# Optimization experiments

Measured on AMD Instinct MI355X. Metric: run time of the kernel, lower is better.

## Reference

```python
import jax, jax.numpy as jnp
import numpy as np

N = 100000        # n_nodes
E = 1600000       # n_edges (avg degree 16)
D = 64            # latent_dim_S
H = 64            # gcn_hidden_dim
EPS = 1e-5        # BatchNorm1d eps


def setup_inputs() -> dict:
    key = jax.random.key(0)
    ks = jax.random.split(key, 6)
    return {
        "edge_index": jax.random.randint(ks[0], (2, E), 0, N, dtype=jnp.int64),
        "u_S": jax.random.normal(ks[1], (N, D), dtype=jnp.float32),
        # GCNConv 1: latent_dim_S -> gcn_hidden_dim
        "w1": jax.random.normal(ks[2], (D, H), dtype=jnp.float32) / np.sqrt(D).astype(np.float32),
        "b1": jnp.zeros((H,), jnp.float32),
        # BatchNorm1d(H)
        "g1": jnp.ones((H,), jnp.float32),
        "beta1": jnp.zeros((H,), jnp.float32),
        # GCNConv 2: gcn_hidden_dim -> 2
        "w2": jax.random.normal(ks[3], (H, 2), dtype=jnp.float32) / np.sqrt(H).astype(np.float32),
        "b2": jnp.zeros((2,), jnp.float32),
        # BatchNorm1d(2)
        "g2": jnp.ones((2,), jnp.float32),
        "beta2": jnp.zeros((2,), jnp.float32),
    }


def reference(edge_index, u_S, w1, b1, g1, beta1, w2, b2, g2, beta2):
    n = u_S.shape[0]
    # PyG GCNConv: add self-loops, symmetric normalization D^-1/2 A D^-1/2
    loop = jnp.arange(n, dtype=edge_index.dtype)
    src = jnp.concatenate([edge_index[0], loop])  # [E+N]
    dst = jnp.concatenate([edge_index[1], loop])
    deg = jnp.zeros((n,), u_S.dtype).at[dst].add(1.0)   # in-degree incl. self-loop (>=1)
    dinv = jax.lax.rsqrt(deg)
    norm = dinv[src] * dinv[dst]                         # [E+N]

    def gcn_conv(x, w, b):
        h = x @ w                                        # transform first (PyG order)
        msg = h[src] * norm[:, None]                     # gather + scale
        out = jnp.zeros((n, h.shape[1]), h.dtype).at[dst].add(msg)  # scatter-add
        return out + b                                   # bias after aggregation

    def batchnorm(x, g, bt):
        m = x.mean(axis=0)
        v = x.var(axis=0)                                # biased variance (train mode)
        return g * (x - m) * jax.lax.rsqrt(v + EPS) + bt

    s = jax.nn.relu(batchnorm(gcn_conv(u_S, w1, b1), g1, beta1))
    s = batchnorm(gcn_conv(s, w2, b2), g2, beta2)
    # nn.Softmax() on 2D input defaults to dim=1
    return jax.nn.sigmoid(s), jax.nn.softmax(s, axis=1)
```

## Files before the change

### kernel.cpp

```cpp
#include <hip/hip_runtime.h>
#include <hip/hip_fp16.h>

#define N_NODES 100000
#define N_EDGES 1600000
#define BN_EPS 1e-5f

#define NBUCK 256
#define NPB   391
#define BCAP  8192
#define EPB_BIN 4096
#define NBLK_BIN ((N_EDGES + EPB_BIN - 1) / EPB_BIN)

#define OFF_GCUR   0
#define OFF_CNT    256
#define OFF_DINV   100352
#define OFF_OFFS   200448
#define OFF_EBUF   300544
#define OFF_STATS1 2397696
#define OFF_STATS2 2397824
#define OFF_HS1    2398016
#define OFF_BINNED OFF_HS1
#define OFF_OUT1   5598016
#define OFF_HS2    8798016
#define OFF_OUT2   8998016

typedef _Float16 f16x8 __attribute__((ext_vector_type(8)));
typedef float    f32x4 __attribute__((ext_vector_type(4)));

__device__ inline float4 cvt4(uint2 v) {
    __half2 a = *(__half2*)&v.x, b = *(__half2*)&v.y;
    float2 fa = __half22float2(a), fb = __half22float2(b);
    return make_float4(fa.x, fa.y, fb.x, fb.y);
}

__global__ __launch_bounds__(256) void k0_init(int* __restrict__ gcur,
                                               float* __restrict__ stats) {
    int t = threadIdx.x;
    gcur[t] = t * BCAP;
    if (t < 132) stats[t] = 0.f;
}

__global__ __launch_bounds__(256) void k_bin(
        const int* __restrict__ src, const int* __restrict__ dst,
        int* __restrict__ gcur, int* __restrict__ binned) {
    __shared__ int hist[NBUCK];
    __shared__ int lcur[NBUCK];
    int t = threadIdx.x, b = blockIdx.x;
    hist[t] = 0;
    __syncthreads();
    int e0 = b * EPB_BIN;
    int pkreg[16], bkreg[16];
#pragma unroll
    for (int i = 0; i < 16; ++i) {
        int e = e0 + t + i * 256;
        if (e < N_EDGES) {
            int s = src[e], d = dst[e];
            int bk = d / NPB;
            bkreg[i] = bk;
            pkreg[i] = s | ((d - bk * NPB) << 17);
            atomicAdd(&hist[bk], 1);
        } else bkreg[i] = -1;
    }
    __syncthreads();
    int h = hist[t];
    lcur[t] = (h > 0) ? atomicAdd(&gcur[t], h) : 0;
    __syncthreads();
#pragma unroll
    for (int i = 0; i < 16; ++i) {
        if (bkreg[i] >= 0) {
            int bk = bkreg[i];
            int pos = atomicAdd(&lcur[bk], 1);
            if (pos < (bk + 1) * BCAP)
                binned[pos] = pkreg[i];
        }
    }
}

__global__ __launch_bounds__(256) void k_csr(
        const int* __restrict__ gcur, const int* __restrict__ binned,
        int* __restrict__ cnt, float* __restrict__ dinv,
        int* __restrict__ offs, int* __restrict__ ebuf) {
    int b = blockIdx.x, t = threadIdx.x;
    int nb0 = b * NPB;
    int nn = min(NPB, N_NODES - nb0);
    __shared__ int lcnt[NPB];
    __shared__ int lcur[NPB];
    __shared__ int sc[512];
    for (int i = t; i < NPB; i += 256) lcnt[i] = 0;
    __syncthreads();
    int base = b * BCAP;
    int m = min(gcur[b] - base, BCAP);
    for (int j = t; j < m; j += 256)
        atomicAdd(&lcnt[((unsigned)binned[base + j]) >> 17], 1);
    __syncthreads();
    sc[t] = (t < NPB) ? lcnt[t] : 0;
    sc[256 + t] = (256 + t < NPB) ? lcnt[256 + t] : 0;
    __syncthreads();
    for (int off = 1; off < 512; off <<= 1) {
        int v0 = (t >= off) ? sc[t - off] : 0;
        int i1 = t + 256;
        int v1 = (i1 >= off) ? sc[i1 - off] : 0;
        __syncthreads();
        sc[t] += v0; sc[i1] += v1;
        __syncthreads();
    }
    for (int i = t; i < nn; i += 256) {
        int c = lcnt[i];
        int excl = sc[i] - c;
        lcur[i] = excl;
        offs[nb0 + i] = base + excl;
        cnt[nb0 + i] = c;
        dinv[nb0 + i] = rsqrtf((float)(1 + c));
    }
    __syncthreads();
    for (int j = t; j < m; j += 256) {
        unsigned v = (unsigned)binned[base + j];
        int pos = atomicAdd(&lcur[v >> 17], 1);
        ebuf[base + pos] = (int)(v & 0x1FFFFu);
    }
}

__global__ __launch_bounds__(256) void k3_xw1(
        const float* __restrict__ u, const float* __restrict__ w1g,
        const float* __restrict__ dinv, __half* __restrict__ hs1) {
    int t = threadIdx.x;
    int lane = t & 63, wid = t >> 6;
    int g = blockIdx.x * 4 + wid;
    if (g >= N_NODES / 16) return;
    int r = lane & 15, kb = lane >> 4;

    f16x8 bf[4][2];
#pragma unroll
    for (int ct = 0; ct < 4; ++ct) {
#pragma unroll
        for (int kh = 0; kh < 2; ++kh) {
            int c = ct * 16 + r;
            int k0 = kh * 32 + kb * 8;
            f16x8 b;
#pragma unroll
            for (int i = 0; i < 8; ++i) b[i] = (_Float16)w1g[(k0 + i) * 64 + c];
            bf[ct][kh] = b;
        }
    }

    const float* up = u + (size_t)g * 16 * 64;
    f16x8 af[2];
#pragma unroll
    for (int kh = 0; kh < 2; ++kh) {
        const float* p = up + r * 64 + kh * 32 + kb * 8;
        float4 v0 = *(const float4*)p;
        float4 v1 = *(const float4*)(p + 4);
        f16x8 a;
        a[0] = (_Float16)v0.x; a[1] = (_Float16)v0.y;
        a[2] = (_Float16)v0.z; a[3] = (_Float16)v0.w;
        a[4] = (_Float16)v1.x; a[5] = (_Float16)v1.y;
        a[6] = (_Float16)v1.z; a[7] = (_Float16)v1.w;
        af[kh] = a;
    }

    f32x4 acc[4];
#pragma unroll
    for (int ct = 0; ct < 4; ++ct) { acc[ct][0]=0.f; acc[ct][1]=0.f; acc[ct][2]=0.f; acc[ct][3]=0.f; }
#pragma unroll
    for (int ct = 0; ct < 4; ++ct) {
        acc[ct] = __builtin_amdgcn_mfma_f32_16x16x32_f16(af[0], bf[ct][0], acc[ct], 0, 0, 0);
        acc[ct] = __builtin_amdgcn_mfma_f32_16x16x32_f16(af[1], bf[ct][1], acc[ct], 0, 0, 0);
    }

    int r0 = g * 16;
    float4 dv = *(const float4*)&dinv[r0 + kb * 4];
    float dvv[4] = {dv.x, dv.y, dv.z, dv.w};
#pragma unroll
    for (int ct = 0; ct < 4; ++ct) {
#pragma unroll
        for (int reg = 0; reg < 4; ++reg) {
            int row = r0 + kb * 4 + reg;
            int col = ct * 16 + r;
            hs1[(size_t)row * 64 + col] = __float2half(acc[ct][reg] * dvv[reg]);
        }
    }
}

__global__ __launch_bounds__(256) void k_pull1(
        const int* __restrict__ offs, const int* __restrict__ cnt,
        const int* __restrict__ ebuf, const float* __restrict__ dinv,
        const __half* __restrict__ hs1, __half* __restrict__ out1) {
    int idx = blockIdx.x * blockDim.x + threadIdx.x;
    int d = idx >> 4, sub = idx & 15;
    if (d >= N_NODES) return;
    const uint2* h4 = (const uint2*)hs1;
    float4 acc = cvt4(h4[d * 16 + sub]);
    int base = offs[d], c = cnt[d];
    if (c > 0) {
        int s = ebuf[base];
        int j = 0;
        for (; j + 1 < c; ++j) {
            int s2 = ebuf[base + j + 1];
            float4 v = cvt4(h4[s * 16 + sub]);
            acc.x += v.x; acc.y += v.y; acc.z += v.z; acc.w += v.w;
            s = s2;
        }
        float4 v = cvt4(h4[s * 16 + sub]);
        acc.x += v.x; acc.y += v.y; acc.z += v.z; acc.w += v.w;
    }
    float di = dinv[d];
    __half2 lo = __floats2half2_rn(acc.x * di, acc.y * di);
    __half2 hi = __floats2half2_rn(acc.z * di, acc.w * di);
    uint2 o; o.x = *(unsigned*)&lo; o.y = *(unsigned*)&hi;
    ((uint2*)out1)[d * 16 + sub] = o;
}

__global__ __launch_bounds__(256) void k5_stats1(
        const __half* __restrict__ out1, float* __restrict__ stats) {
    int tid = blockIdx.x * blockDim.x + threadIdx.x;
    int gsz = gridDim.x * blockDim.x;
    const uint4* p = (const uint4*)out1;
    const int total = N_NODES * 8;
    float s[8], q[8];
#pragma unroll
    for (int j = 0; j < 8; ++j) { s[j] = 0.f; q[j] = 0.f; }
    for (int i = tid; i < total; i += gsz) {
        uint4 v = p[i];
        unsigned w[4] = {v.x, v.y, v.z, v.w};
#pragma unroll
        for (int h = 0; h < 4; ++h) {
            float2 f = __half22float2(*(__half2*)&w[h]);
            s[2*h]   += f.x; q[2*h]   = fmaf(f.x, f.x, q[2*h]);
            s[2*h+1] += f.y; q[2*h+1] = fmaf(f.y, f.y, q[2*h+1]);
        }
    }
#pragma unroll
    for (int m = 8; m < 64; m <<= 1) {
#pragma unroll
        for (int j = 0; j < 8; ++j) {
            s[j] += __shfl_xor(s[j], m);
            q[j] += __shfl_xor(q[j], m);
        }
    }
    __shared__ float red[4][128];
    int lane = threadIdx.x & 63, wv = threadIdx.x >> 6;
    if (lane < 8) {
        int c0 = lane * 8;
#pragma unroll
        for (int j = 0; j < 8; ++j) {
            red[wv][c0 + j] = s[j];
            red[wv][64 + c0 + j] = q[j];
        }
    }
    __syncthreads();
    if (threadIdx.x < 128) {
        int t = threadIdx.x;
        float v = red[0][t] + red[1][t] + red[2][t] + red[3][t];
        unsafeAtomicAdd(&stats[t], v);
    }
}

__global__ __launch_bounds__(256) void k7_xw2(
        const __half* __restrict__ out1, const float* __restrict__ stats,
        const float* __restrict__ g1, const float* __restrict__ beta1,
        const float* __restrict__ w2, const float* __restrict__ dinv,
        float* __restrict__ hs2) {
    __shared__ float lsc[64], lsh[64];
    int c = threadIdx.x & 63;
    int wv = threadIdx.x >> 6;
    if (threadIdx.x < 64) {
        float invn = 1.f / (float)N_NODES;
        float m = stats[c] * invn;
        float v = stats[64 + c] * invn - m * m;
        float inv = rsqrtf(v + BN_EPS);
        float sc = g1[c] * inv;
        lsc[c] = sc;
        lsh[c] = beta1[c] - m * sc;
    }
    __syncthreads();
    float s0 = lsc[c], h0 = lsh[c];
    float w20 = w2[c * 2], w21 = w2[c * 2 + 1];
    int stride = gridDim.x * 4;
    for (int r = blockIdx.x * 4 + wv; r < N_NODES; r += stride) {
        float x = __half2float(out1[r * 64 + c]);
        float y = fmaxf(fmaf(x, s0, h0), 0.f);
        float p0 = y * w20, p1 = y * w21;
#pragma unroll
        for (int m = 32; m; m >>= 1) {
            p0 += __shfl_xor(p0, m);
            p1 += __shfl_xor(p1, m);
        }
        if (c == 0) {
            float di = dinv[r];
            hs2[r * 2] = p0 * di;
            hs2[r * 2 + 1] = p1 * di;
        }
    }
}

__global__ __launch_bounds__(256) void k_pull2(
        const int* __restrict__ offs, const int* __restrict__ cnt,
        const int* __restrict__ ebuf, const float* __restrict__ dinv,
        const float* __restrict__ hs2, float* __restrict__ out2,
        float* __restrict__ stats2) {
    int d = blockIdx.x * blockDim.x + threadIdx.x;
    float o0 = 0.f, o1 = 0.f;
    if (d < N_NODES) {
        const float2* h2 = (const float2*)hs2;
        float2 self = h2[d];
        o0 = self.x; o1 = self.y;
        int base = offs[d], c = cnt[d];
        for (int j = 0; j < c; ++j) {
            int s = ebuf[base + j];
            float2 v = h2[s];
            o0 += v.x; o1 += v.y;
        }
        float di = dinv[d];
        o0 *= di; o1 *= di;
        ((float2*)out2)[d] = make_float2(o0, o1);
    }
    float s0 = o0, s1 = o1, q0 = o0 * o0, q1 = o1 * o1;
#pragma unroll
    for (int m = 32; m; m >>= 1) {
        s0 += __shfl_down(s0, m); s1 += __shfl_down(s1, m);
        q0 += __shfl_down(q0, m); q1 += __shfl_down(q1, m);
    }
    __shared__ float red[4][4];
    int wv = threadIdx.x >> 6;
    if ((threadIdx.x & 63) == 0) {
        red[0][wv] = s0; red[1][wv] = s1; red[2][wv] = q0; red[3][wv] = q1;
    }
    __syncthreads();
    if (threadIdx.x < 4) {
        int i = threadIdx.x;
        float v = red[i][0] + red[i][1] + red[i][2] + red[i][3];
        unsafeAtomicAdd(&stats2[i], v);
    }
}

__global__ __launch_bounds__(256) void k10_head(
        const float* __restrict__ out2, const float* __restrict__ stats2,
        const float* __restrict__ g2, const float* __restrict__ beta2,
        float* __restrict__ out) {
    int r = blockIdx.x * blockDim.x + threadIdx.x;
    if (r >= N_NODES) return;
    float invn = 1.f / (float)N_NODES;
    float m0 = stats2[0] * invn, m1 = stats2[1] * invn;
    float v0 = stats2[2] * invn - m0 * m0;
    float v1 = stats2[3] * invn - m1 * m1;
    float i0 = rsqrtf(v0 + BN_EPS), i1 = rsqrtf(v1 + BN_EPS);
    float sc0 = g2[0] * i0, sc1 = g2[1] * i1;
    float sh0 = beta2[0] - m0 * sc0, sh1 = beta2[1] - m1 * sc1;
    float2 x = ((const float2*)out2)[r];
    float y0 = fmaf(x.x, sc0, sh0), y1 = fmaf(x.y, sc1, sh1);
    out[r * 2] = 1.f / (1.f + __expf(-y0));
    out[r * 2 + 1] = 1.f / (1.f + __expf(-y1));
    out[2 * N_NODES + r * 2] = 1.f / (1.f + __expf(y1 - y0));
    out[2 * N_NODES + r * 2 + 1] = 1.f / (1.f + __expf(y0 - y1));
}

extern "C" void kernel_launch(void* const* d_in, const int* in_sizes, int n_in,
                              void* d_out, int out_size, void* d_ws, size_t ws_size,
                              hipStream_t stream) {
    const int*   edge  = (const int*)d_in[0];
    const float* u_S   = (const float*)d_in[1];
    const float* w1    = (const float*)d_in[2];
    const float* g1    = (const float*)d_in[4];
    const float* beta1 = (const float*)d_in[5];
    const float* w2    = (const float*)d_in[6];
    const float* g2    = (const float*)d_in[8];
    const float* beta2 = (const float*)d_in[9];
    float* out = (float*)d_out;

    float*  ws     = (float*)d_ws;
    int*    gcur   = (int*)(ws + OFF_GCUR);
    int*    cnt    = (int*)(ws + OFF_CNT);
    float*  dinv   = ws + OFF_DINV;
    int*    offs   = (int*)(ws + OFF_OFFS);
    int*    ebuf   = (int*)(ws + OFF_EBUF);
    float*  stats1 = ws + OFF_STATS1;
    float*  stats2 = ws + OFF_STATS2;
    __half* hs1    = (__half*)(ws + OFF_HS1);
    int*    binned = (int*)(ws + OFF_BINNED);
    __half* out1   = (__half*)(ws + OFF_OUT1);
    float*  hs2    = ws + OFF_HS2;
    float*  out2   = ws + OFF_OUT2;

    const int* src = edge;
    const int* dst = edge + N_EDGES;

    k0_init<<<1, 256, 0, stream>>>(gcur, stats1);
    k_bin<<<NBLK_BIN, 256, 0, stream>>>(src, dst, gcur, binned);
    k_csr<<<NBUCK, 256, 0, stream>>>(gcur, binned, cnt, dinv, offs, ebuf);
    k3_xw1<<<(N_NODES / 16 + 3) / 4, 256, 0, stream>>>(u_S, w1, dinv, hs1);
    k_pull1<<<(N_NODES * 16 + 255) / 256, 256, 0, stream>>>(offs, cnt, ebuf, dinv, hs1, out1);
    k5_stats1<<<256, 256, 0, stream>>>(out1, stats1);
    k7_xw2<<<2048, 256, 0, stream>>>(out1, stats1, g1, beta1, w2, dinv, hs2);
    k_pull2<<<(N_NODES + 255) / 256, 256, 0, stream>>>(offs, cnt, ebuf, dinv, hs2, out2, stats2);
    k10_head<<<(N_NODES + 255) / 256, 256, 0, stream>>>(out2, stats2, g2, beta2, out);
}
```

Before: 227.7 us.

## Fuse BN1 statistics into pull1, unroll gathers, and use MFMA for second linear

```diff
diff --git a/kernel.cpp b/kernel.cpp
--- a/kernel.cpp
+++ b/kernel.cpp
@@ -10,6 +10,9 @@
 #define BCAP  8192
 #define EPB_BIN 4096
 #define NBLK_BIN ((N_EDGES + EPB_BIN - 1) / EPB_BIN)
+
+#define P1_NBLK 512
+#define K7_NBLK 512
 
 #define OFF_GCUR   0
 #define OFF_CNT    256
@@ -184,74 +187,68 @@
 __global__ __launch_bounds__(256) void k_pull1(
         const int* __restrict__ offs, const int* __restrict__ cnt,
         const int* __restrict__ ebuf, const float* __restrict__ dinv,
-        const __half* __restrict__ hs1, __half* __restrict__ out1) {
-    int idx = blockIdx.x * blockDim.x + threadIdx.x;
-    int d = idx >> 4, sub = idx & 15;
-    if (d >= N_NODES) return;
+        const __half* __restrict__ hs1, __half* __restrict__ out1,
+        float* __restrict__ stats) {
     const uint2* h4 = (const uint2*)hs1;
-    float4 acc = cvt4(h4[d * 16 + sub]);
-    int base = offs[d], c = cnt[d];
-    if (c > 0) {
-        int s = ebuf[base];
+    int sub = threadIdx.x & 15;
+    int stride = gridDim.x * blockDim.x;
+    float ps[4] = {0.f, 0.f, 0.f, 0.f};
+    float pq[4] = {0.f, 0.f, 0.f, 0.f};
+    for (int idx = blockIdx.x * blockDim.x + threadIdx.x; idx < N_NODES * 16;
+         idx += stride) {
+        int d = idx >> 4;
+        float4 acc = cvt4(h4[d * 16 + sub]);
+        int base = offs[d], c = cnt[d];
         int j = 0;
-        for (; j + 1 < c; ++j) {
-            int s2 = ebuf[base + j + 1];
-            float4 v = cvt4(h4[s * 16 + sub]);
+        for (; j + 4 <= c; j += 4) {
+            int s0 = ebuf[base + j],     s1 = ebuf[base + j + 1];
+            int s2 = ebuf[base + j + 2], s3 = ebuf[base + j + 3];
+            float4 v0 = cvt4(h4[s0 * 16 + sub]);
+            float4 v1 = cvt4(h4[s1 * 16 + sub]);
+            float4 v2 = cvt4(h4[s2 * 16 + sub]);
+            float4 v3 = cvt4(h4[s3 * 16 + sub]);
+            acc.x += (v0.x + v1.x) + (v2.x + v3.x);
+            acc.y += (v0.y + v1.y) + (v2.y + v3.y);
+            acc.z += (v0.z + v1.z) + (v2.z + v3.z);
+            acc.w += (v0.w + v1.w) + (v2.w + v3.w);
+        }
+        for (; j < c; ++j) {
+            float4 v = cvt4(h4[ebuf[base + j] * 16 + sub]);
             acc.x += v.x; acc.y += v.y; acc.z += v.z; acc.w += v.w;
-            s = s2;
-        }
-        float4 v = cvt4(h4[s * 16 + sub]);
-        acc.x += v.x; acc.y += v.y; acc.z += v.z; acc.w += v.w;
-    }
-    float di = dinv[d];
-    __half2 lo = __floats2half2_rn(acc.x * di, acc.y * di);
-    __half2 hi = __floats2half2_rn(acc.z * di, acc.w * di);
-    uint2 o; o.x = *(unsigned*)&lo; o.y = *(unsigned*)&hi;
-    ((uint2*)out1)[d * 16 + sub] = o;
-}
-
-__global__ __launch_bounds__(256) void k5_stats1(
-        const __half* __restrict__ out1, float* __restrict__ stats) {
-    int tid = blockIdx.x * blockDim.x + threadIdx.x;
-    int gsz = gridDim.x * blockDim.x;
-    const uint4* p = (const uint4*)out1;
-    const int total = N_NODES * 8;
-    float s[8], q[8];
-#pragma unroll
-    for (int j = 0; j < 8; ++j) { s[j] = 0.f; q[j] = 0.f; }
-    for (int i = tid; i < total; i += gsz) {
-        uint4 v = p[i];
-        unsigned w[4] = {v.x, v.y, v.z, v.w};
-#pragma unroll
-        for (int h = 0; h < 4; ++h) {
-            float2 f = __half22float2(*(__half2*)&w[h]);
-            s[2*h]   += f.x; q[2*h]   = fmaf(f.x, f.x, q[2*h]);
-            s[2*h+1] += f.y; q[2*h+1] = fmaf(f.y, f.y, q[2*h+1]);
-        }
-    }
-#pragma unroll
-    for (int m = 8; m < 64; m <<= 1) {
-#pragma unroll
-        for (int j = 0; j < 8; ++j) {
-            s[j] += __shfl_xor(s[j], m);
-            q[j] += __shfl_xor(q[j], m);
+        }
+        float di = dinv[d];
+        acc.x *= di; acc.y *= di; acc.z *= di; acc.w *= di;
+        __half2 lo = __floats2half2_rn(acc.x, acc.y);
+        __half2 hi = __floats2half2_rn(acc.z, acc.w);
+        uint2 o; o.x = *(unsigned*)&lo; o.y = *(unsigned*)&hi;
+        ((uint2*)out1)[d * 16 + sub] = o;
+        ps[0] += acc.x; pq[0] = fmaf(acc.x, acc.x, pq[0]);
+        ps[1] += acc.y; pq[1] = fmaf(acc.y, acc.y, pq[1]);
+        ps[2] += acc.z; pq[2] = fmaf(acc.z, acc.z, pq[2]);
+        ps[3] += acc.w; pq[3] = fmaf(acc.w, acc.w, pq[3]);
+    }
+#pragma unroll
+    for (int m = 16; m < 64; m <<= 1) {
+#pragma unroll
+        for (int jj = 0; jj < 4; ++jj) {
+            ps[jj] += __shfl_xor(ps[jj], m);
+            pq[jj] += __shfl_xor(pq[jj], m);
         }
     }
     __shared__ float red[4][128];
     int lane = threadIdx.x & 63, wv = threadIdx.x >> 6;
-    if (lane < 8) {
-        int c0 = lane * 8;
-#pragma unroll
-        for (int j = 0; j < 8; ++j) {
-            red[wv][c0 + j] = s[j];
-            red[wv][64 + c0 + j] = q[j];
+    if (lane < 16) {
+#pragma unroll
+        for (int jj = 0; jj < 4; ++jj) {
+            red[wv][lane * 4 + jj] = ps[jj];
+            red[wv][64 + lane * 4 + jj] = pq[jj];
         }
     }
     __syncthreads();
     if (threadIdx.x < 128) {
-        int t = threadIdx.x;
-        float v = red[0][t] + red[1][t] + red[2][t] + red[3][t];
-        unsafeAtomicAdd(&stats[t], v);
+        int tt = threadIdx.x;
+        float v = red[0][tt] + red[1][tt] + red[2][tt] + red[3][tt];
+        unsafeAtomicAdd(&stats[tt], v);
     }
 }
 
@@ -261,34 +258,60 @@
         const float* __restrict__ w2, const float* __restrict__ dinv,
         float* __restrict__ hs2) {
     __shared__ float lsc[64], lsh[64];
-    int c = threadIdx.x & 63;
-    int wv = threadIdx.x >> 6;
-    if (threadIdx.x < 64) {
+    int t = threadIdx.x;
+    if (t < 64) {
         float invn = 1.f / (float)N_NODES;
-        float m = stats[c] * invn;
-        float v = stats[64 + c] * invn - m * m;
+        float m = stats[t] * invn;
+        float v = stats[64 + t] * invn - m * m;
         float inv = rsqrtf(v + BN_EPS);
-        float sc = g1[c] * inv;
-        lsc[c] = sc;
-        lsh[c] = beta1[c] - m * sc;
-    }
-    __syncthreads();
-    float s0 = lsc[c], h0 = lsh[c];
-    float w20 = w2[c * 2], w21 = w2[c * 2 + 1];
-    int stride = gridDim.x * 4;
-    for (int r = blockIdx.x * 4 + wv; r < N_NODES; r += stride) {
-        float x = __half2float(out1[r * 64 + c]);
-        float y = fmaxf(fmaf(x, s0, h0), 0.f);
-        float p0 = y * w20, p1 = y * w21;
-#pragma unroll
-        for (int m = 32; m; m >>= 1) {
-            p0 += __shfl_xor(p0, m);
-            p1 += __shfl_xor(p1, m);
-        }
-        if (c == 0) {
-            float di = dinv[r];
-            hs2[r * 2] = p0 * di;
-            hs2[r * 2 + 1] = p1 * di;
+        float sc = g1[t] * inv;
+        lsc[t] = sc;
+        lsh[t] = beta1[t] - m * sc;
+    }
+    __syncthreads();
+    int lane = t & 63, wv = t >> 6;
+    int r = lane & 15, kb = lane >> 4;
+    f16x8 bf[2];
+    float scr[2][8], shr[2][8];
+#pragma unroll
+    for (int kh = 0; kh < 2; ++kh) {
+        int k0 = kh * 32 + kb * 8;
+        f16x8 b;
+#pragma unroll
+        for (int i = 0; i < 8; ++i) {
+            b[i] = (r < 2) ? (_Float16)w2[(k0 + i) * 2 + r] : (_Float16)0.f;
+            scr[kh][i] = lsc[k0 + i];
+            shr[kh][i] = lsh[k0 + i];
+        }
+        bf[kh] = b;
+    }
+    const int NGRP = N_NODES / 16;
+    int wid = blockIdx.x * 4 + wv;
+    for (int g = wid; g < NGRP; g += K7_NBLK * 4) {
+        f32x4 acc; acc[0]=0.f; acc[1]=0.f; acc[2]=0.f; acc[3]=0.f;
+#pragma unroll
+        for (int kh = 0; kh < 2; ++kh) {
+            uint4 av = *(const uint4*)(out1 + (size_t)(g * 16 + r) * 64 + kh * 32 + kb * 8);
+            unsigned w[4] = {av.x, av.y, av.z, av.w};
+            f16x8 a;
+#pragma unroll
+            for (int h = 0; h < 4; ++h) {
+                float2 f = __half22float2(*(__half2*)&w[h]);
+                float y0 = fmaxf(fmaf(f.x, scr[kh][2*h],   shr[kh][2*h]),   0.f);
+                float y1 = fmaxf(fmaf(f.y, scr[kh][2*h+1], shr[kh][2*h+1]), 0.f);
+                a[2*h]   = (_Float16)y0;
+                a[2*h+1] = (_Float16)y1;
+            }
+            acc = __builtin_amdgcn_mfma_f32_16x16x32_f16(a, bf[kh], acc, 0, 0, 0);
+        }
+        if (r < 2) {
+            float4 dv = *(const float4*)&dinv[g * 16 + kb * 4];
+            float dvv[4] = {dv.x, dv.y, dv.z, dv.w};
+#pragma unroll
+            for (int reg = 0; reg < 4; ++reg) {
+                int row = g * 16 + kb * 4 + reg;
+                hs2[row * 2 + r] = acc[reg] * dvv[reg];
+            }
         }
     }
 }
@@ -388,9 +411,8 @@
     k_bin<<<NBLK_BIN, 256, 0, stream>>>(src, dst, gcur, binned);
     k_csr<<<NBUCK, 256, 0, stream>>>(gcur, binned, cnt, dinv, offs, ebuf);
     k3_xw1<<<(N_NODES / 16 + 3) / 4, 256, 0, stream>>>(u_S, w1, dinv, hs1);
-    k_pull1<<<(N_NODES * 16 + 255) / 256, 256, 0, stream>>>(offs, cnt, ebuf, dinv, hs1, out1);
-    k5_stats1<<<256, 256, 0, stream>>>(out1, stats1);
-    k7_xw2<<<2048, 256, 0, stream>>>(out1, stats1, g1, beta1, w2, dinv, hs2);
+    k_pull1<<<P1_NBLK, 256, 0, stream>>>(offs, cnt, ebuf, dinv, hs1, out1, stats1);
+    k7_xw2<<<K7_NBLK, 256, 0, stream>>>(out1, stats1, g1, beta1, w2, dinv, hs2);
     k_pull2<<<(N_NODES + 255) / 256, 256, 0, stream>>>(offs, cnt, ebuf, dinv, hs2, out2, stats2);
     k10_head<<<(N_NODES + 255) / 256, 256, 0, stream>>>(out2, stats2, g2, beta2, out);
 }
```

New measurement: 244.7 us. 1.07x slower.

## Widen pull1 gathers to 16-byte loads and run layer-2 transform on MFMA

Applied to the files above, without the earlier changes.

```diff
diff --git a/kernel.cpp b/kernel.cpp
--- a/kernel.cpp
+++ b/kernel.cpp
@@ -10,6 +10,8 @@
 #define BCAP  8192
 #define EPB_BIN 4096
 #define NBLK_BIN ((N_EDGES + EPB_BIN - 1) / EPB_BIN)
+
+#define K7_NBLK 1563
 
 #define OFF_GCUR   0
 #define OFF_CNT    256
@@ -27,10 +29,13 @@
 typedef _Float16 f16x8 __attribute__((ext_vector_type(8)));
 typedef float    f32x4 __attribute__((ext_vector_type(4)));
 
-__device__ inline float4 cvt4(uint2 v) {
-    __half2 a = *(__half2*)&v.x, b = *(__half2*)&v.y;
-    float2 fa = __half22float2(a), fb = __half22float2(b);
-    return make_float4(fa.x, fa.y, fb.x, fb.y);
+__device__ inline void cvt8(uint4 v, float* f) {
+    float2 a = __half22float2(*(__half2*)&v.x);
+    float2 b = __half22float2(*(__half2*)&v.y);
+    float2 c = __half22float2(*(__half2*)&v.z);
+    float2 d = __half22float2(*(__half2*)&v.w);
+    f[0] = a.x; f[1] = a.y; f[2] = b.x; f[3] = b.y;
+    f[4] = c.x; f[5] = c.y; f[6] = d.x; f[7] = d.y;
 }
 
 __global__ __launch_bounds__(256) void k0_init(int* __restrict__ gcur,
@@ -186,28 +191,37 @@
         const int* __restrict__ ebuf, const float* __restrict__ dinv,
         const __half* __restrict__ hs1, __half* __restrict__ out1) {
     int idx = blockIdx.x * blockDim.x + threadIdx.x;
-    int d = idx >> 4, sub = idx & 15;
+    int d = idx >> 3, sub = idx & 7;
     if (d >= N_NODES) return;
-    const uint2* h4 = (const uint2*)hs1;
-    float4 acc = cvt4(h4[d * 16 + sub]);
+    const uint4* h8 = (const uint4*)hs1;
+    float acc[8];
+    cvt8(h8[d * 8 + sub], acc);
     int base = offs[d], c = cnt[d];
     if (c > 0) {
         int s = ebuf[base];
         int j = 0;
         for (; j + 1 < c; ++j) {
             int s2 = ebuf[base + j + 1];
-            float4 v = cvt4(h4[s * 16 + sub]);
-            acc.x += v.x; acc.y += v.y; acc.z += v.z; acc.w += v.w;
+            float v[8];
+            cvt8(h8[s * 8 + sub], v);
+#pragma unroll
+            for (int k = 0; k < 8; ++k) acc[k] += v[k];
             s = s2;
         }
-        float4 v = cvt4(h4[s * 16 + sub]);
-        acc.x += v.x; acc.y += v.y; acc.z += v.z; acc.w += v.w;
+        float v[8];
+        cvt8(h8[s * 8 + sub], v);
+#pragma unroll
+        for (int k = 0; k < 8; ++k) acc[k] += v[k];
     }
     float di = dinv[d];
-    __half2 lo = __floats2half2_rn(acc.x * di, acc.y * di);
-    __half2 hi = __floats2half2_rn(acc.z * di, acc.w * di);
-    uint2 o; o.x = *(unsigned*)&lo; o.y = *(unsigned*)&hi;
-    ((uint2*)out1)[d * 16 + sub] = o;
+    __half2 p0 = __floats2half2_rn(acc[0] * di, acc[1] * di);
+    __half2 p1 = __floats2half2_rn(acc[2] * di, acc[3] * di);
+    __half2 p2 = __floats2half2_rn(acc[4] * di, acc[5] * di);
+    __half2 p3 = __floats2half2_rn(acc[6] * di, acc[7] * di);
+    uint4 o;
+    o.x = *(unsigned*)&p0; o.y = *(unsigned*)&p1;
+    o.z = *(unsigned*)&p2; o.w = *(unsigned*)&p3;
+    ((uint4*)out1)[d * 8 + sub] = o;
 }
 
 __global__ __launch_bounds__(256) void k5_stats1(
@@ -261,34 +275,60 @@
         const float* __restrict__ w2, const float* __restrict__ dinv,
         float* __restrict__ hs2) {
     __shared__ float lsc[64], lsh[64];
-    int c = threadIdx.x & 63;
-    int wv = threadIdx.x >> 6;
-    if (threadIdx.x < 64) {
+    int t = threadIdx.x;
+    if (t < 64) {
         float invn = 1.f / (float)N_NODES;
-        float m = stats[c] * invn;
-        float v = stats[64 + c] * invn - m * m;
+        float m = stats[t] * invn;
+        float v = stats[64 + t] * invn - m * m;
         float inv = rsqrtf(v + BN_EPS);
-        float sc = g1[c] * inv;
-        lsc[c] = sc;
-        lsh[c] = beta1[c] - m * sc;
-    }
-    __syncthreads();
-    float s0 = lsc[c], h0 = lsh[c];
-    float w20 = w2[c * 2], w21 = w2[c * 2 + 1];
-    int stride = gridDim.x * 4;
-    for (int r = blockIdx.x * 4 + wv; r < N_NODES; r += stride) {
-        float x = __half2float(out1[r * 64 + c]);
-        float y = fmaxf(fmaf(x, s0, h0), 0.f);
-        float p0 = y * w20, p1 = y * w21;
-#pragma unroll
-        for (int m = 32; m; m >>= 1) {
-            p0 += __shfl_xor(p0, m);
-            p1 += __shfl_xor(p1, m);
-        }
-        if (c == 0) {
-            float di = dinv[r];
-            hs2[r * 2] = p0 * di;
-            hs2[r * 2 + 1] = p1 * di;
+        float sc = g1[t] * inv;
+        lsc[t] = sc;
+        lsh[t] = beta1[t] - m * sc;
+    }
+    __syncthreads();
+    int lane = t & 63, wv = t >> 6;
+    int r = lane & 15, kb = lane >> 4;
+    f16x8 bf[2];
+    float scr[2][8], shr[2][8];
+#pragma unroll
+    for (int kh = 0; kh < 2; ++kh) {
+        int k0 = kh * 32 + kb * 8;
+        f16x8 b;
+#pragma unroll
+        for (int i = 0; i < 8; ++i) {
+            b[i] = (r < 2) ? (_Float16)w2[(k0 + i) * 2 + r] : (_Float16)0.f;
+            scr[kh][i] = lsc[k0 + i];
+            shr[kh][i] = lsh[k0 + i];
+        }
+        bf[kh] = b;
+    }
+    const int NGRP = N_NODES / 16;
+    int wid = blockIdx.x * 4 + wv;
+    for (int g = wid; g < NGRP; g += K7_NBLK * 4) {
+        f32x4 acc; acc[0]=0.f; acc[1]=0.f; acc[2]=0.f; acc[3]=0.f;
+#pragma unroll
+        for (int kh = 0; kh < 2; ++kh) {
+            uint4 av = *(const uint4*)(out1 + (size_t)(g * 16 + r) * 64 + kh * 32 + kb * 8);
+            unsigned w[4] = {av.x, av.y, av.z, av.w};
+            f16x8 a;
+#pragma unroll
+            for (int h = 0; h < 4; ++h) {
+                float2 f = __half22float2(*(__half2*)&w[h]);
+                float y0 = fmaxf(fmaf(f.x, scr[kh][2*h],   shr[kh][2*h]),   0.f);
+                float y1 = fmaxf(fmaf(f.y, scr[kh][2*h+1], shr[kh][2*h+1]), 0.f);
+                a[2*h]   = (_Float16)y0;
+                a[2*h+1] = (_Float16)y1;
+            }
+            acc = __builtin_amdgcn_mfma_f32_16x16x32_f16(a, bf[kh], acc, 0, 0, 0);
+        }
+        if (r < 2) {
+            float4 dv = *(const float4*)&dinv[g * 16 + kb * 4];
+            float dvv[4] = {dv.x, dv.y, dv.z, dv.w};
+#pragma unroll
+            for (int reg = 0; reg < 4; ++reg) {
+                int row = g * 16 + kb * 4 + reg;
+                hs2[row * 2 + r] = acc[reg] * dvv[reg];
+            }
         }
     }
 }
@@ -388,9 +428,9 @@
     k_bin<<<NBLK_BIN, 256, 0, stream>>>(src, dst, gcur, binned);
     k_csr<<<NBUCK, 256, 0, stream>>>(gcur, binned, cnt, dinv, offs, ebuf);
     k3_xw1<<<(N_NODES / 16 + 3) / 4, 256, 0, stream>>>(u_S, w1, dinv, hs1);
-    k_pull1<<<(N_NODES * 16 + 255) / 256, 256, 0, stream>>>(offs, cnt, ebuf, dinv, hs1, out1);
+    k_pull1<<<(N_NODES * 8 + 255) / 256, 256, 0, stream>>>(offs, cnt, ebuf, dinv, hs1, out1);
     k5_stats1<<<256, 256, 0, stream>>>(out1, stats1);
-    k7_xw2<<<2048, 256, 0, stream>>>(out1, stats1, g1, beta1, w2, dinv, hs2);
+    k7_xw2<<<K7_NBLK, 256, 0, stream>>>(out1, stats1, g1, beta1, w2, dinv, hs2);
     k_pull2<<<(N_NODES + 255) / 256, 256, 0, stream>>>(offs, cnt, ebuf, dinv, hs2, out2, stats2);
     k10_head<<<(N_NODES + 255) / 256, 256, 0, stream>>>(out2, stats2, g2, beta2, out);
 }
```

New measurement: 211.1 us. 7.3% less time.
